# Optimization experiments

Measured on AMD Instinct MI355X. Metric: run time of the kernel, lower is better.

Reference implementation:

```python
import jax, jax.numpy as jnp
import numpy as np

B, N, T, FM = 2, 768, 96, 8
HID = 64
TD = HID // 2   # temporal_dim = max(8, 32) = 32
MD = HID // 2   # mark_hidden_dim = 32


def _lin_init(key, fan_in, fan_out):
    k1, k2 = jax.random.split(key)
    bound = 1.0 / np.sqrt(fan_in)
    w = jax.random.uniform(k1, (fan_in, fan_out), minval=-bound, maxval=bound, dtype=jnp.float32)
    b = jax.random.uniform(k2, (fan_out,), minval=-bound, maxval=bound, dtype=jnp.float32)
    return w, b


def setup_inputs() -> dict:
    key = jax.random.key(0)
    ks = jax.random.split(key, 16)
    x_hist = jax.random.normal(ks[0], (B, N, T), dtype=jnp.float32)
    x_mark = jax.random.normal(ks[1], (B, N, T, FM), dtype=jnp.float32)
    a_static = jax.random.uniform(ks[2], (N, N), dtype=jnp.float32)
    te_w1, te_b1 = _lin_init(ks[3], 3, TD)
    te_w2, te_b2 = _lin_init(ks[4], TD, TD)
    me_w1, me_b1 = _lin_init(ks[5], FM, MD)
    me_w2, me_b2 = _lin_init(ks[6], MD, MD)
    nf_w, nf_b = _lin_init(ks[7], TD + MD, HID)
    ps_w1, ps_b1 = _lin_init(ks[8], 3 * HID, HID)
    ps_w2, ps_b2 = _lin_init(ks[9], HID, 1)
    raw_lambda = jnp.array([np.log(0.1 / 0.9)], dtype=jnp.float32)  # logit(lambda_init)
    return dict(x_hist=x_hist, x_mark=x_mark, a_static=a_static,
                te_w1=te_w1, te_b1=te_b1, te_w2=te_w2, te_b2=te_b2,
                me_w1=me_w1, me_b1=me_b1, me_w2=me_w2, me_b2=me_b2,
                nf_w=nf_w, nf_b=nf_b,
                ps_w1=ps_w1, ps_b1=ps_b1, ps_w2=ps_w2, ps_b2=ps_b2,
                raw_lambda=raw_lambda)


def reference(x_hist, x_mark, a_static,
              te_w1, te_b1, te_w2, te_b2,
              me_w1, me_b1, me_w2, me_b2,
              nf_w, nf_b, ps_w1, ps_b1, ps_w2, ps_b2, raw_lambda):
    n = x_hist.shape[1]
    # temporal stats: last / mean / max over T -> [B,N,3]
    stats = jnp.stack([x_hist[:, :, -1], x_hist.mean(axis=-1), x_hist.max(axis=-1)], axis=-1)
    h_t = jax.nn.relu(stats @ te_w1 + te_b1) @ te_w2 + te_b2          # [B,N,TD]
    mark_sum = x_mark.mean(axis=2)                                    # [B,N,FM]
    h_m = jax.nn.relu(mark_sum @ me_w1 + me_b1) @ me_w2 + me_b2       # [B,N,MD]
    h = jax.nn.relu(jnp.concatenate([h_t, h_m], axis=-1) @ nf_w + nf_b)  # [B,N,H]
    # pair scorer: Linear([h_i, h_j, |h_i-h_j|]) decomposed over the 3 blocks
    hdim = h.shape[-1]
    w_i, w_j, w_d = ps_w1[:hdim], ps_w1[hdim:2 * hdim], ps_w1[2 * hdim:]
    s_i = h @ w_i                                                     # [B,N,H]
    s_j = h @ w_j                                                     # [B,N,H]
    diff = jnp.abs(h[:, :, None, :] - h[:, None, :, :])               # [B,N,N,H]
    pre = s_i[:, :, None, :] + s_j[:, None, :, :] + diff @ w_d + ps_b1
    delta = jnp.tanh((jax.nn.relu(pre) @ ps_w2 + ps_b2)[..., 0])      # [B,N,N]
    eye = jnp.eye(n, dtype=delta.dtype)
    delta = delta * (1.0 - eye)
    delta = 0.5 * (delta + jnp.swapaxes(delta, 1, 2))                 # sym_graph
    lam = jax.nn.sigmoid(raw_lambda)                                  # [1]
    a_hybrid = a_static[None] + lam * delta
    a_hybrid = jax.nn.relu(a_hybrid)                                  # nonneg_mode='relu'
    d = jnp.clip(a_hybrid.sum(axis=-1, keepdims=True), 1e-6, None)    # row norm
    a_hybrid = a_hybrid / d
    return a_hybrid, lam
```

## Files before the change

### kernel.cpp

```cpp
#include <hip/hip_runtime.h>
#include <hip/hip_bf16.h>
#include <math.h>

#define B_ 2
#define N_ 768
#define T_ 96
#define FM_ 8
#define HID_ 64
#define TD_ 32
#define MD_ 32
#define TILE 16
#define TI32 32
#define NTILES (N_/TILE)
#define PERB 600
#define SJSTR 66

typedef __attribute__((ext_vector_type(8))) short short8v;
typedef __attribute__((ext_vector_type(4))) float f32x4;
typedef __attribute__((ext_vector_type(2))) float f32x2;
typedef __attribute__((ext_vector_type(4))) unsigned int uint4v;

__device__ __forceinline__ unsigned int pack_bf2(float d0, float d1){
  __hip_bfloat162 t = __float22bfloat162_rn(make_float2(d0, d1));
  unsigned int u;
  __builtin_memcpy(&u, &t, 4);
  return u;
}

__device__ __forceinline__ float ftanh(float x){
  float e = __expf(2.f * x);
  return 1.f - 2.f * __builtin_amdgcn_rcpf(e + 1.f);
}

__device__ __forceinline__ float wave_sum64(float v){
  #pragma unroll
  for (int m = 32; m; m >>= 1) v += __shfl_xor(v, m);
  return v;
}
__device__ __forceinline__ float wave_max64(float v){
  #pragma unroll
  for (int m = 32; m; m >>= 1) v = fmaxf(v, __shfl_xor(v, m));
  return v;
}

__global__ __launch_bounds__(256) void feat_kernel(
    const float* __restrict__ x_hist, const float* __restrict__ x_mark,
    const float* __restrict__ te_w1, const float* __restrict__ te_b1,
    const float* __restrict__ te_w2, const float* __restrict__ te_b2,
    const float* __restrict__ me_w1, const float* __restrict__ me_b1,
    const float* __restrict__ me_w2, const float* __restrict__ me_b2,
    const float* __restrict__ nf_w,  const float* __restrict__ nf_b,
    const float* __restrict__ ps_w1,
    float* __restrict__ h_out, float* __restrict__ si_out, float* __restrict__ sj_out,
    unsigned short* __restrict__ wdf)
{
  const int tid  = threadIdx.x;
  const int lane = tid & 63;
  const int w    = tid >> 6;
  const int NB   = (B_ * N_) / 4;

  if (blockIdx.x >= NB) {
    const int q  = (blockIdx.x - NB) * 4 + w;
    const int nt = q >> 1, s = q & 1;
    const int col = (lane & 15) + 16 * nt;
    const int k0  = s * 32 + ((lane >> 4) << 3);
    #pragma unroll
    for (int jj = 0; jj < 8; ++jj) {
      float v = ps_w1[(2 * HID_ + k0 + jj) * HID_ + col];
      __hip_bfloat16 bv = __float2bfloat16(v);
      unsigned short us;
      __builtin_memcpy(&us, &bv, 2);
      wdf[(q * 64 + lane) * 8 + jj] = us;
    }
    return;
  }

  const int row = blockIdx.x * 4 + w;

  __shared__ float st [4][3];
  __shared__ float ms [4][FM_];
  __shared__ float t1s[4][TD_];
  __shared__ float m1s[4][MD_];
  __shared__ float hc [4][HID_];
  __shared__ float hs [4][HID_];

  const float* xh = x_hist + (long)row * T_;
  float s  = xh[lane];
  float mx = s;
  if (lane < T_ - 64) { float v = xh[lane + 64]; s += v; mx = fmaxf(mx, v); }
  s  = wave_sum64(s);
  mx = wave_max64(mx);
  if (lane == 0) { st[w][0] = xh[T_ - 1]; st[w][1] = s * (1.0f / T_); st[w][2] = mx; }

  const float* xm = x_mark + (long)row * T_ * FM_;
  float msv = 0.f;
  #pragma unroll
  for (int k = 0; k < 12; ++k) msv += xm[lane + 64 * k];
  msv += __shfl_xor(msv, 8);
  msv += __shfl_xor(msv, 16);
  msv += __shfl_xor(msv, 32);
  if (lane < FM_) ms[w][lane] = msv * (1.0f / T_);
  __syncthreads();

  if (lane < TD_) {
    float a = te_b1[lane];
    #pragma unroll
    for (int k = 0; k < 3; ++k) a += st[w][k] * te_w1[k * TD_ + lane];
    t1s[w][lane] = fmaxf(a, 0.f);
    float am = me_b1[lane];
    #pragma unroll
    for (int k = 0; k < FM_; ++k) am += ms[w][k] * me_w1[k * MD_ + lane];
    m1s[w][lane] = fmaxf(am, 0.f);
  }
  __syncthreads();
  if (lane < TD_) {
    float a = te_b2[lane];
    #pragma unroll
    for (int k = 0; k < TD_; ++k) a += t1s[w][k] * te_w2[k * TD_ + lane];
    hc[w][lane] = a;
    float am = me_b2[lane];
    #pragma unroll
    for (int k = 0; k < MD_; ++k) am += m1s[w][k] * me_w2[k * MD_ + lane];
    hc[w][TD_ + lane] = am;
  }
  __syncthreads();
  {
    float a = nf_b[lane];
    #pragma unroll
    for (int k = 0; k < HID_; ++k) a += hc[w][k] * nf_w[k * HID_ + lane];
    float hv = fmaxf(a, 0.f);
    hs[w][lane] = hv;
    h_out[(long)row * HID_ + lane] = hv;
  }
  __syncthreads();
  {
    float a1 = 0.f, a2 = 0.f;
    #pragma unroll
    for (int k = 0; k < HID_; ++k) {
      float hv = hs[w][k];
      a1 += hv * ps_w1[k * HID_ + lane];
      a2 += hv * ps_w1[(HID_ + k) * HID_ + lane];
    }
    si_out[(long)row * HID_ + lane] = a1;
    sj_out[(long)row * HID_ + lane] = a2;
  }
}

__global__ __launch_bounds__(256, 3) void pair_kernel(
    const float* __restrict__ h, const float* __restrict__ si, const float* __restrict__ sj,
    const float* __restrict__ ps_b1, const float* __restrict__ ps_w2,
    const float* __restrict__ ps_b2, const unsigned short* __restrict__ wdf,
    float* __restrict__ delta)
{
  int bidx = blockIdx.x;
  int b = bidx / PERB;
  int t = bidx % PERB;
  int a = 0;
  while (t >= NTILES - 2 * a) { t -= NTILES - 2 * a; ++a; }
  int tJ = 2 * a + t;
  const int i0 = a * TI32, j0 = tJ * TILE;

  __shared__ float hI  [TI32][HID_];
  __shared__ float hJT [HID_][TILE + 1];
  __shared__ f32x2 SI2 [TI32][HID_];
  __shared__ f32x2 SJ2 [TILE][SJSTR];

  const int tid  = threadIdx.x;
  const int lane = tid & 63;
  const int w    = tid >> 6;

  {
    const int r  = tid >> 4;
    const int c4 = (tid & 15) * 4;
    const f32x4 b14 = *(const f32x4*)(ps_b1 + c4);
    #pragma unroll
    for (int p = 0; p < 2; ++p) {
      const int rr = r + p * 16;
      const long gi = ((long)b * N_ + i0 + rr) * HID_ + c4;
      *(f32x4*)&hI[rr][c4] = *(const f32x4*)(h + gi);
      f32x4 vii = *(const f32x4*)(si + gi) + b14;
      f32x4 vji = *(const f32x4*)(sj + gi);
      #pragma unroll
      for (int q = 0; q < 4; ++q) SI2[rr][c4 + q] = (f32x2){vii[q], vji[q]};
    }
    const long gj = ((long)b * N_ + j0 + r) * HID_ + c4;
    f32x4 vhj = *(const f32x4*)(h + gj);
    #pragma unroll
    for (int q = 0; q < 4; ++q) hJT[c4 + q][r] = vhj[q];
    f32x4 vij = *(const f32x4*)(si + gj) + b14;
    f32x4 vjj = *(const f32x4*)(sj + gj);
    #pragma unroll
    for (int q = 0; q < 4; ++q) SJ2[r][c4 + q] = (f32x2){vjj[q], vij[q]};
  }
  const float b2 = ps_b2[0];
  __syncthreads();

  const int g   = lane >> 4;
  const int c16 = lane & 15;

  short8v wfr[8];
  const short8v* wdp = (const short8v*)wdf;
  #pragma unroll
  for (int q = 0; q < 8; ++q) wfr[q] = wdp[q * 64 + lane];

  float hJv[2][8];
  #pragma unroll
  for (int s = 0; s < 2; ++s)
    #pragma unroll
    for (int jj = 0; jj < 8; ++jj)
      hJv[s][jj] = hJT[32 * s + 8 * g + jj][c16];

  f32x2 sJ2h[16];
  float w2h[16];
  #pragma unroll
  for (int mt = 0; mt < 4; ++mt) {
    const int cb = 16 * mt + 4 * g;
    f32x4 u0 = *(const f32x4*)&SJ2[c16][cb];
    f32x4 u1 = *(const f32x4*)&SJ2[c16][cb + 2];
    sJ2h[mt*4+0] = (f32x2){u0[0], u0[1]};
    sJ2h[mt*4+1] = (f32x2){u0[2], u0[3]};
    sJ2h[mt*4+2] = (f32x2){u1[0], u1[1]};
    sJ2h[mt*4+3] = (f32x2){u1[2], u1[3]};
    #pragma unroll
    for (int r = 0; r < 4; ++r) w2h[mt*4+r] = ps_w2[cb + r];
  }

  float* drow = delta + (long)b * N_ * N_;

  #pragma unroll
  for (int m = 0; m < 8; ++m) {
    const int iloc = w * 8 + m;
    const int i = i0 + iloc;

    short8v afr[2];
    #pragma unroll
    for (int s = 0; s < 2; ++s) {
      f32x4 ha = *(const f32x4*)&hI[iloc][32 * s + 8 * g];
      f32x4 hb = *(const f32x4*)&hI[iloc][32 * s + 8 * g + 4];
      uint4v uv;
      #pragma unroll
      for (int p = 0; p < 2; ++p) {
        float d0 = fabsf(ha[2*p]   - hJv[s][2*p]);
        float d1 = fabsf(ha[2*p+1] - hJv[s][2*p+1]);
        uv[p] = pack_bf2(d0, d1);
      }
      #pragma unroll
      for (int p = 0; p < 2; ++p) {
        float d0 = fabsf(hb[2*p]   - hJv[s][4 + 2*p]);
        float d1 = fabsf(hb[2*p+1] - hJv[s][4 + 2*p+1]);
        uv[2 + p] = pack_bf2(d0, d1);
      }
      afr[s] = __builtin_bit_cast(short8v, uv);
    }

    f32x4 acc[4];
    #pragma unroll
    for (int mt = 0; mt < 4; ++mt) acc[mt] = (f32x4){0.f, 0.f, 0.f, 0.f};
    #pragma unroll
    for (int s = 0; s < 2; ++s)
      #pragma unroll
      for (int mt = 0; mt < 4; ++mt)
        acc[mt] = __builtin_amdgcn_mfma_f32_16x16x32_bf16(wfr[2 * mt + s], afr[s], acc[mt], 0, 0, 0);

    f32x2 acc2 = (f32x2){0.f, 0.f};
    #pragma unroll
    for (int mt = 0; mt < 4; ++mt) {
      const int cb = 16 * mt + 4 * g;
      f32x4 s01 = *(const f32x4*)&SI2[iloc][cb];
      f32x4 s23 = *(const f32x4*)&SI2[iloc][cb + 2];
      #pragma unroll
      for (int r = 0; r < 4; ++r) {
        f32x2 siv = (r < 2) ? (f32x2){s01[2*r], s01[2*r+1]}
                            : (f32x2){s23[2*(r-2)], s23[2*(r-2)+1]};
        float av = acc[mt][r];
        f32x2 pre = siv + sJ2h[mt*4+r];
        pre = pre + (f32x2){av, av};
        pre = __builtin_elementwise_max(pre, (f32x2){0.f, 0.f});
        acc2 = acc2 + pre * (f32x2){w2h[mt*4+r], w2h[mt*4+r]};
      }
    }
    float a1 = acc2[0], a2 = acc2[1];
    a1 += __shfl_xor(a1, 16);  a1 += __shfl_xor(a1, 32);
    a2 += __shfl_xor(a2, 16);  a2 += __shfl_xor(a2, 32);

    if (g == 0) {
      const int j = j0 + c16;
      if (i < j) {
        float sym = 0.5f * (ftanh(a1 + b2) + ftanh(a2 + b2));
        drow[(long)i * N_ + j] = sym;
        drow[(long)j * N_ + i] = sym;
      } else if (i == j) {
        drow[(long)i * N_ + i] = 0.f;
      }
    }
  }
}

__global__ __launch_bounds__(256) void norm_kernel(
    const float* __restrict__ a_static, const float* __restrict__ raw_lambda,
    float* __restrict__ out)
{
  const int row = blockIdx.x;
  const int i   = row % N_;
  const int tid = threadIdx.x;
  const float lam = 1.f / (1.f + expf(-raw_lambda[0]));

  const float* arow = a_static + (long)i * N_;
  float* drow = out + (long)row * N_;

  float vals[3];
  float s = 0.f;
  #pragma unroll
  for (int r = 0; r < 3; ++r) {
    int j = r * 256 + tid;
    float v = arow[j] + lam * drow[j];
    v = fmaxf(v, 0.f);
    vals[r] = v;
    s += v;
  }
  s = wave_sum64(s);
  __shared__ float ps[4];
  if ((tid & 63) == 0) ps[tid >> 6] = s;
  __syncthreads();
  float tot = ps[0] + ps[1] + ps[2] + ps[3];
  float inv = 1.f / fmaxf(tot, 1e-6f);
  #pragma unroll
  for (int r = 0; r < 3; ++r) {
    int j = r * 256 + tid;
    drow[j] = vals[r] * inv;
  }
  if (row == 0 && tid == 0) out[(long)B_ * N_ * N_] = lam;
}

extern "C" void kernel_launch(void* const* d_in, const int* in_sizes, int n_in,
                              void* d_out, int out_size, void* d_ws, size_t ws_size,
                              hipStream_t stream) {
  const float* x_hist     = (const float*)d_in[0];
  const float* x_mark     = (const float*)d_in[1];
  const float* a_static   = (const float*)d_in[2];
  const float* te_w1      = (const float*)d_in[3];
  const float* te_b1      = (const float*)d_in[4];
  const float* te_w2      = (const float*)d_in[5];
  const float* te_b2      = (const float*)d_in[6];
  const float* me_w1      = (const float*)d_in[7];
  const float* me_b1      = (const float*)d_in[8];
  const float* me_w2      = (const float*)d_in[9];
  const float* me_b2      = (const float*)d_in[10];
  const float* nf_w       = (const float*)d_in[11];
  const float* nf_b       = (const float*)d_in[12];
  const float* ps_w1      = (const float*)d_in[13];
  const float* ps_b1      = (const float*)d_in[14];
  const float* ps_w2      = (const float*)d_in[15];
  const float* ps_b2      = (const float*)d_in[16];
  const float* raw_lambda = (const float*)d_in[17];

  float* out = (float*)d_out;
  float* h   = (float*)d_ws;
  float* si  = h  + (long)B_ * N_ * HID_;
  float* sj  = si + (long)B_ * N_ * HID_;
  unsigned short* wdf = (unsigned short*)(sj + (long)B_ * N_ * HID_);

  feat_kernel<<<(B_ * N_) / 4 + 2, 256, 0, stream>>>(
      x_hist, x_mark, te_w1, te_b1, te_w2, te_b2,
      me_w1, me_b1, me_w2, me_b2, nf_w, nf_b, ps_w1, h, si, sj, wdf);

  pair_kernel<<<B_ * PERB, 256, 0, stream>>>(
      h, si, sj, ps_b1, ps_w2, ps_b2, wdf, out);

  norm_kernel<<<B_ * N_, 256, 0, stream>>>(a_static, raw_lambda, out);
}
```

Before: 36.62 us.

## Replace abs-diff with bf16 min via |a-b| = a+b-2min(a,b)

Since h is non-negative after ReLU, the kernel rewrites |h_i-h_j|·W_d as h_i·W_d + h_j·W_d − 2·min(h_i,h_j)·W_d. The per-node terms are folded into the precomputed si/sj, which are now stored packed as float2. The pair loop then takes the elementwise min directly on bf16 bit patterns, which order like unsigned integers for non-negative values. This removes the per-pair subtract, abs and fp32-to-bf16 conversions. h is also stored in bf16 to cut global and LDS traffic, and the occupancy hint rises from 3 to 4 blocks. In exchange, rounding h to bf16 before the min changes numerics slightly versus the old order of subtract then round.

```diff
diff --git a/kernel.cpp b/kernel.cpp
--- a/kernel.cpp
+++ b/kernel.cpp
@@ -13,19 +13,11 @@
 #define TI32 32
 #define NTILES (N_/TILE)
 #define PERB 600
-#define SJSTR 66
 
 typedef __attribute__((ext_vector_type(8))) short short8v;
+typedef __attribute__((ext_vector_type(8))) unsigned short ushort8v;
 typedef __attribute__((ext_vector_type(4))) float f32x4;
 typedef __attribute__((ext_vector_type(2))) float f32x2;
-typedef __attribute__((ext_vector_type(4))) unsigned int uint4v;
-
-__device__ __forceinline__ unsigned int pack_bf2(float d0, float d1){
-  __hip_bfloat162 t = __float22bfloat162_rn(make_float2(d0, d1));
-  unsigned int u;
-  __builtin_memcpy(&u, &t, 4);
-  return u;
-}
 
 __device__ __forceinline__ float ftanh(float x){
   float e = __expf(2.f * x);
@@ -51,7 +43,7 @@
     const float* __restrict__ me_w2, const float* __restrict__ me_b2,
     const float* __restrict__ nf_w,  const float* __restrict__ nf_b,
     const float* __restrict__ ps_w1,
-    float* __restrict__ h_out, float* __restrict__ si_out, float* __restrict__ sj_out,
+    unsigned short* __restrict__ hbf, f32x2* __restrict__ siq,
     unsigned short* __restrict__ wdf)
 {
   const int tid  = threadIdx.x;
@@ -130,24 +122,29 @@
     for (int k = 0; k < HID_; ++k) a += hc[w][k] * nf_w[k * HID_ + lane];
     float hv = fmaxf(a, 0.f);
     hs[w][lane] = hv;
-    h_out[(long)row * HID_ + lane] = hv;
+    __hip_bfloat16 hb = __float2bfloat16(hv);
+    unsigned short us;
+    __builtin_memcpy(&us, &hb, 2);
+    hbf[(long)row * HID_ + lane] = us;
   }
   __syncthreads();
   {
-    float a1 = 0.f, a2 = 0.f;
+    float a1 = 0.f, a2 = 0.f, u = 0.f;
     #pragma unroll
     for (int k = 0; k < HID_; ++k) {
       float hv = hs[w][k];
       a1 += hv * ps_w1[k * HID_ + lane];
       a2 += hv * ps_w1[(HID_ + k) * HID_ + lane];
-    }
-    si_out[(long)row * HID_ + lane] = a1;
-    sj_out[(long)row * HID_ + lane] = a2;
-  }
-}
-
-__global__ __launch_bounds__(256, 3) void pair_kernel(
-    const float* __restrict__ h, const float* __restrict__ si, const float* __restrict__ sj,
+      float wv = ps_w1[(2 * HID_ + k) * HID_ + lane];
+      __hip_bfloat16 wb = __float2bfloat16(wv);
+      u += hv * __bfloat162float(wb);
+    }
+    siq[(long)row * HID_ + lane] = (f32x2){a1 + u, a2 + u};
+  }
+}
+
+__global__ __launch_bounds__(256, 4) void pair_kernel(
+    const unsigned short* __restrict__ hbf, const f32x2* __restrict__ siq,
     const float* __restrict__ ps_b1, const float* __restrict__ ps_w2,
     const float* __restrict__ ps_b2, const unsigned short* __restrict__ wdf,
     float* __restrict__ delta)
@@ -160,37 +157,39 @@
   int tJ = 2 * a + t;
   const int i0 = a * TI32, j0 = tJ * TILE;
 
-  __shared__ float hI  [TI32][HID_];
-  __shared__ float hJT [HID_][TILE + 1];
-  __shared__ f32x2 SI2 [TI32][HID_];
-  __shared__ f32x2 SJ2 [TILE][SJSTR];
+  __shared__ unsigned short hIbf[TI32][HID_];
+  __shared__ unsigned short hJbf[TILE][72];
+  __shared__ f32x2 SI2[TI32][HID_];
+  __shared__ f32x2 SJ2[TILE][66];
 
   const int tid  = threadIdx.x;
   const int lane = tid & 63;
   const int w    = tid >> 6;
 
   {
-    const int r  = tid >> 4;
-    const int c4 = (tid & 15) * 4;
-    const f32x4 b14 = *(const f32x4*)(ps_b1 + c4);
-    #pragma unroll
-    for (int p = 0; p < 2; ++p) {
-      const int rr = r + p * 16;
-      const long gi = ((long)b * N_ + i0 + rr) * HID_ + c4;
-      *(f32x4*)&hI[rr][c4] = *(const f32x4*)(h + gi);
-      f32x4 vii = *(const f32x4*)(si + gi) + b14;
-      f32x4 vji = *(const f32x4*)(sj + gi);
-      #pragma unroll
-      for (int q = 0; q < 4; ++q) SI2[rr][c4 + q] = (f32x2){vii[q], vji[q]};
-    }
-    const long gj = ((long)b * N_ + j0 + r) * HID_ + c4;
-    f32x4 vhj = *(const f32x4*)(h + gj);
-    #pragma unroll
-    for (int q = 0; q < 4; ++q) hJT[c4 + q][r] = vhj[q];
-    f32x4 vij = *(const f32x4*)(si + gj) + b14;
-    f32x4 vjj = *(const f32x4*)(sj + gj);
-    #pragma unroll
-    for (int q = 0; q < 4; ++q) SJ2[r][c4 + q] = (f32x2){vjj[q], vij[q]};
+    const int r8 = tid >> 3;
+    const int ch = tid & 7;
+    const long gri = (long)(b * N_ + i0 + r8) * HID_;
+    *(ushort8v*)&hIbf[r8][8 * ch] = *(const ushort8v*)(hbf + gri + 8 * ch);
+    const f32x4* sp = (const f32x4*)(siq + gri + 8 * ch);
+    f32x4* dp = (f32x4*)&SI2[r8][8 * ch];
+    dp[0] = sp[0]; dp[1] = sp[1]; dp[2] = sp[2]; dp[3] = sp[3];
+
+    if (tid < 128) {
+      const int rj = tid >> 3;
+      const long grj = (long)(b * N_ + j0 + rj) * HID_;
+      *(ushort8v*)&hJbf[rj][8 * ch] = *(const ushort8v*)(hbf + grj + 8 * ch);
+      const f32x4* sj = (const f32x4*)(siq + grj + 8 * ch);
+      const f32x4 b4a = *(const f32x4*)(ps_b1 + 8 * ch);
+      const f32x4 b4b = *(const f32x4*)(ps_b1 + 8 * ch + 4);
+      f32x4 v0 = sj[0], v1 = sj[1], v2 = sj[2], v3 = sj[3];
+      f32x4 o0 = {v0[1] + b4a[0], v0[0] + b4a[0], v0[3] + b4a[1], v0[2] + b4a[1]};
+      f32x4 o1 = {v1[1] + b4a[2], v1[0] + b4a[2], v1[3] + b4a[3], v1[2] + b4a[3]};
+      f32x4 o2 = {v2[1] + b4b[0], v2[0] + b4b[0], v2[3] + b4b[1], v2[2] + b4b[1]};
+      f32x4 o3 = {v3[1] + b4b[2], v3[0] + b4b[2], v3[3] + b4b[3], v3[2] + b4b[3]};
+      f32x4* dj = (f32x4*)&SJ2[rj][8 * ch];
+      dj[0] = o0; dj[1] = o1; dj[2] = o2; dj[3] = o3;
+    }
   }
   const float b2 = ps_b2[0];
   __syncthreads();
@@ -203,15 +202,10 @@
   #pragma unroll
   for (int q = 0; q < 8; ++q) wfr[q] = wdp[q * 64 + lane];
 
-  float hJv[2][8];
-  #pragma unroll
-  for (int s = 0; s < 2; ++s)
-    #pragma unroll
-    for (int jj = 0; jj < 8; ++jj)
-      hJv[s][jj] = hJT[32 * s + 8 * g + jj][c16];
-
+  ushort8v hj0 = *(const ushort8v*)&hJbf[c16][8 * g];
+  ushort8v hj1 = *(const ushort8v*)&hJbf[c16][32 + 8 * g];
   f32x2 sJ2h[16];
-  float w2h[16];
+  f32x4 w24[4];
   #pragma unroll
   for (int mt = 0; mt < 4; ++mt) {
     const int cb = 16 * mt + 4 * g;
@@ -221,8 +215,7 @@
     sJ2h[mt*4+1] = (f32x2){u0[2], u0[3]};
     sJ2h[mt*4+2] = (f32x2){u1[0], u1[1]};
     sJ2h[mt*4+3] = (f32x2){u1[2], u1[3]};
-    #pragma unroll
-    for (int r = 0; r < 4; ++r) w2h[mt*4+r] = ps_w2[cb + r];
+    w24[mt] = *(const f32x4*)(ps_w2 + cb);
   }
 
   float* drow = delta + (long)b * N_ * N_;
@@ -232,35 +225,19 @@
     const int iloc = w * 8 + m;
     const int i = i0 + iloc;
 
-    short8v afr[2];
-    #pragma unroll
-    for (int s = 0; s < 2; ++s) {
-      f32x4 ha = *(const f32x4*)&hI[iloc][32 * s + 8 * g];
-      f32x4 hb = *(const f32x4*)&hI[iloc][32 * s + 8 * g + 4];
-      uint4v uv;
-      #pragma unroll
-      for (int p = 0; p < 2; ++p) {
-        float d0 = fabsf(ha[2*p]   - hJv[s][2*p]);
-        float d1 = fabsf(ha[2*p+1] - hJv[s][2*p+1]);
-        uv[p] = pack_bf2(d0, d1);
-      }
-      #pragma unroll
-      for (int p = 0; p < 2; ++p) {
-        float d0 = fabsf(hb[2*p]   - hJv[s][4 + 2*p]);
-        float d1 = fabsf(hb[2*p+1] - hJv[s][4 + 2*p+1]);
-        uv[2 + p] = pack_bf2(d0, d1);
-      }
-      afr[s] = __builtin_bit_cast(short8v, uv);
-    }
+    ushort8v hi0 = *(const ushort8v*)&hIbf[iloc][8 * g];
+    ushort8v hi1 = *(const ushort8v*)&hIbf[iloc][32 + 8 * g];
+    short8v af0 = __builtin_bit_cast(short8v, __builtin_elementwise_min(hi0, hj0));
+    short8v af1 = __builtin_bit_cast(short8v, __builtin_elementwise_min(hi1, hj1));
 
     f32x4 acc[4];
     #pragma unroll
     for (int mt = 0; mt < 4; ++mt) acc[mt] = (f32x4){0.f, 0.f, 0.f, 0.f};
     #pragma unroll
-    for (int s = 0; s < 2; ++s)
-      #pragma unroll
-      for (int mt = 0; mt < 4; ++mt)
-        acc[mt] = __builtin_amdgcn_mfma_f32_16x16x32_bf16(wfr[2 * mt + s], afr[s], acc[mt], 0, 0, 0);
+    for (int mt = 0; mt < 4; ++mt) {
+      acc[mt] = __builtin_amdgcn_mfma_f32_16x16x32_bf16(wfr[2 * mt + 0], af0, acc[mt], 0, 0, 0);
+      acc[mt] = __builtin_amdgcn_mfma_f32_16x16x32_bf16(wfr[2 * mt + 1], af1, acc[mt], 0, 0, 0);
+    }
 
     f32x2 acc2 = (f32x2){0.f, 0.f};
     #pragma unroll
@@ -274,9 +251,10 @@
                             : (f32x2){s23[2*(r-2)], s23[2*(r-2)+1]};
         float av = acc[mt][r];
         f32x2 pre = siv + sJ2h[mt*4+r];
-        pre = pre + (f32x2){av, av};
+        pre = pre + (f32x2){-2.f * av, -2.f * av};
         pre = __builtin_elementwise_max(pre, (f32x2){0.f, 0.f});
-        acc2 = acc2 + pre * (f32x2){w2h[mt*4+r], w2h[mt*4+r]};
+        f32x2 w22 = (f32x2){w24[mt][r], w24[mt][r]};
+        acc2 = acc2 + pre * w22;
       }
     }
     float a1 = acc2[0], a2 = acc2[1];
@@ -355,17 +333,17 @@
   const float* raw_lambda = (const float*)d_in[17];
 
   float* out = (float*)d_out;
-  float* h   = (float*)d_ws;
-  float* si  = h  + (long)B_ * N_ * HID_;
-  float* sj  = si + (long)B_ * N_ * HID_;
-  unsigned short* wdf = (unsigned short*)(sj + (long)B_ * N_ * HID_);
+  char* ws = (char*)d_ws;
+  unsigned short* hbf = (unsigned short*)ws;
+  f32x2* siq          = (f32x2*)(ws + 196608);
+  unsigned short* wdf = (unsigned short*)(ws + 196608 + 786432);
 
   feat_kernel<<<(B_ * N_) / 4 + 2, 256, 0, stream>>>(
       x_hist, x_mark, te_w1, te_b1, te_w2, te_b2,
-      me_w1, me_b1, me_w2, me_b2, nf_w, nf_b, ps_w1, h, si, sj, wdf);
+      me_w1, me_b1, me_w2, me_b2, nf_w, nf_b, ps_w1, hbf, siq, wdf);
 
   pair_kernel<<<B_ * PERB, 256, 0, stream>>>(
-      h, si, sj, ps_b1, ps_w2, ps_b2, wdf, out);
+      hbf, siq, ps_b1, ps_w2, ps_b2, wdf, out);
 
   norm_kernel<<<B_ * N_, 256, 0, stream>>>(a_static, raw_lambda, out);
 }
```

After: 48.39 us. 1.32x slower.
